# Kernel optimization log

Hardware: AMD Instinct MI355X
Metric: run time of the kernel (lower is better)

The kernel has to match this reference:

```python
import jax, jax.numpy as jnp
import numpy as np
import math

B, S, DIM = 32, 1, 4096
NH, NKV, HD = 32, 8, 128
MAXLEN = 4096
START_POS = 4095


def _rope(t, freqs):
    # t: (b, s, h, hd); freqs: (s, hd//2, 2) = (cos/real, sin/imag)
    b, s, h, hd = t.shape
    tr = t.astype(jnp.float32).reshape(b, s, h, hd // 2, 2)
    c = freqs[None, :, None, :, 0]
    sn = freqs[None, :, None, :, 1]
    x0, x1 = tr[..., 0], tr[..., 1]
    out = jnp.stack([x0 * c - x1 * sn, x0 * sn + x1 * c], axis=-1)
    return out.reshape(b, s, h, hd).astype(t.dtype)


def setup_inputs() -> dict:
    key = jax.random.key(0)
    ks = jax.random.split(key, 8)
    sd = 1.0 / math.sqrt(DIM)
    x = jax.random.normal(ks[0], (B, S, DIM), dtype=jnp.float32)
    freqs = jax.random.normal(ks[1], (S, HD // 2, 2), dtype=jnp.float32)
    cache_k = jax.random.normal(ks[2], (B, MAXLEN, NKV, HD), dtype=jnp.float32)
    cache_v = jax.random.normal(ks[3], (B, MAXLEN, NKV, HD), dtype=jnp.float32)
    wq = jax.random.normal(ks[4], (NH * HD, DIM), dtype=jnp.float32) * sd
    wk = jax.random.normal(ks[5], (NKV * HD, DIM), dtype=jnp.float32) * sd
    wv = jax.random.normal(ks[6], (NKV * HD, DIM), dtype=jnp.float32) * sd
    wo = jax.random.normal(ks[7], (DIM, NH * HD), dtype=jnp.float32) * sd
    return {"x": x, "freqs": freqs, "cache_k": cache_k, "cache_v": cache_v,
            "wq": wq, "wk": wk, "wv": wv, "wo": wo, "start_pos": START_POS}


def reference(x, freqs, cache_k, cache_v, wq, wk, wv, wo, start_pos):
    b, s, _ = x.shape
    n_rep = NH // NKV
    xq = (x @ wq.T).reshape(b, s, NH, HD)
    xk = (x @ wk.T).reshape(b, s, NKV, HD)
    xv = (x @ wv.T).reshape(b, s, NKV, HD)
    xq = _rope(xq, freqs)
    xk = _rope(xk, freqs)
    # KV-cache write then read of prefix (static start_pos)
    keys = cache_k.at[:, start_pos:start_pos + s].set(xk)[:, :start_pos + s]
    values = cache_v.at[:, start_pos:start_pos + s].set(xv)[:, :start_pos + s]
    # GQA: group q heads (g=NKV kv groups, r=n_rep) without materializing repeat
    q = xq.reshape(b, s, NKV, n_rep, HD)
    scores = jnp.einsum('bsgrd,blgd->bgrsl', q, keys) / math.sqrt(HD)
    probs = jax.nn.softmax(scores.astype(jnp.float32), axis=-1).astype(xq.dtype)
    out = jnp.einsum('bgrsl,blgd->bsgrd', probs, values).reshape(b, s, NH * HD)
    return out @ wo.T
```

## Files before the change

kernel.cpp:

```cpp
#include <hip/hip_runtime.h>

#define QSCALE 0.08838834764831845f


#define GEMM_FMA(r, wf) \
    acc[r][0] = fmaf(wf.x, x0.x, acc[r][0]); acc[r][0] = fmaf(wf.y, x0.y, acc[r][0]); \
    acc[r][0] = fmaf(wf.z, x0.z, acc[r][0]); acc[r][0] = fmaf(wf.w, x0.w, acc[r][0]); \
    acc[r][1] = fmaf(wf.x, x1.x, acc[r][1]); acc[r][1] = fmaf(wf.y, x1.y, acc[r][1]); \
    acc[r][1] = fmaf(wf.z, x1.z, acc[r][1]); acc[r][1] = fmaf(wf.w, x1.w, acc[r][1]); \
    acc[r][2] = fmaf(wf.x, x2.x, acc[r][2]); acc[r][2] = fmaf(wf.y, x2.y, acc[r][2]); \
    acc[r][2] = fmaf(wf.z, x2.z, acc[r][2]); acc[r][2] = fmaf(wf.w, x2.w, acc[r][2]); \
    acc[r][3] = fmaf(wf.x, x3.x, acc[r][3]); acc[r][3] = fmaf(wf.y, x3.y, acc[r][3]); \
    acc[r][3] = fmaf(wf.z, x3.z, acc[r][3]); acc[r][3] = fmaf(wf.w, x3.w, acc[r][3]);

__device__ __forceinline__ void gemv3(
    const float* __restrict__ W,
    const float* __restrict__ X,
    float* __restrict__ part, const int M, const int m0, const int ks)
{
    const int t = threadIdx.x;
    const int ksub = t & 3;
    const int ngrp = (t >> 2) & 7;
    const int mgrp = t >> 5;

    const int kbase = ks * 256 + ksub * 4;
    const float* wr0 = W + (size_t)(mgrp * 8 + 0) * 4096 + kbase;
    const float* wr1 = W + (size_t)(mgrp * 8 + 1) * 4096 + kbase;
    const float* wr2 = W + (size_t)(mgrp * 8 + 2) * 4096 + kbase;
    const float* wr3 = W + (size_t)(mgrp * 8 + 3) * 4096 + kbase;
    const float* wr4 = W + (size_t)(mgrp * 8 + 4) * 4096 + kbase;
    const float* wr5 = W + (size_t)(mgrp * 8 + 5) * 4096 + kbase;
    const float* wr6 = W + (size_t)(mgrp * 8 + 6) * 4096 + kbase;
    const float* wr7 = W + (size_t)(mgrp * 8 + 7) * 4096 + kbase;
    const float* xr0 = X + (size_t)(ngrp * 4 + 0) * 4096 + kbase;
    const float* xr1 = X + (size_t)(ngrp * 4 + 1) * 4096 + kbase;
    const float* xr2 = X + (size_t)(ngrp * 4 + 2) * 4096 + kbase;
    const float* xr3 = X + (size_t)(ngrp * 4 + 3) * 4096 + kbase;

    float acc[8][4];
#pragma unroll
    for (int r = 0; r < 8; ++r)
#pragma unroll
        for (int n = 0; n < 4; ++n) acc[r][n] = 0.f;

#pragma unroll 2
    for (int c = 0; c < 16; ++c) {
        const int off = c * 16;
        const float4 w0 = *(const float4*)(wr0 + off);
        const float4 w1 = *(const float4*)(wr1 + off);
        const float4 w2 = *(const float4*)(wr2 + off);
        const float4 w3 = *(const float4*)(wr3 + off);
        const float4 w4 = *(const float4*)(wr4 + off);
        const float4 w5 = *(const float4*)(wr5 + off);
        const float4 w6 = *(const float4*)(wr6 + off);
        const float4 w7 = *(const float4*)(wr7 + off);
        const float4 x0 = *(const float4*)(xr0 + off);
        const float4 x1 = *(const float4*)(xr1 + off);
        const float4 x2 = *(const float4*)(xr2 + off);
        const float4 x3 = *(const float4*)(xr3 + off);
        GEMM_FMA(0, w0) GEMM_FMA(1, w1) GEMM_FMA(2, w2) GEMM_FMA(3, w3)
        GEMM_FMA(4, w4) GEMM_FMA(5, w5) GEMM_FMA(6, w6) GEMM_FMA(7, w7)
    }

#pragma unroll
    for (int r = 0; r < 8; ++r)
#pragma unroll
        for (int n = 0; n < 4; ++n) {
            acc[r][n] += __shfl_xor(acc[r][n], 1);
            acc[r][n] += __shfl_xor(acc[r][n], 2);
        }

    if (ksub == 0) {
        float* base = part + (size_t)ks * 32 * M + m0 + mgrp * 8;
#pragma unroll
        for (int n = 0; n < 4; ++n) {
            float* dst = base + (size_t)(ngrp * 4 + n) * M;
            *(float4*)(dst)     = make_float4(acc[0][n], acc[1][n], acc[2][n], acc[3][n]);
            *(float4*)(dst + 4) = make_float4(acc[4][n], acc[5][n], acc[6][n], acc[7][n]);
        }
    }
}

__global__ __launch_bounds__(256, 4) void gemv_qkv_kernel(
    const float* __restrict__ wq, const float* __restrict__ wk,
    const float* __restrict__ wv, const float* __restrict__ x,
    float* __restrict__ part)
{
    const int mb = blockIdx.x >> 4, ks = blockIdx.x & 15;
    const int m0 = mb * 64;
    const float* W;
    if (m0 < 4096)      W = wq + (size_t)m0 * 4096;
    else if (m0 < 5120) W = wk + (size_t)(m0 - 4096) * 4096;
    else                W = wv + (size_t)(m0 - 5120) * 4096;
    gemv3(W, x, part, 6144, m0, ks);
}

__global__ __launch_bounds__(256, 4) void gemv_out_kernel(
    const float* __restrict__ wo, const float* __restrict__ a_ws,
    float* __restrict__ part)
{
    const int mb = blockIdx.x >> 4, ks = blockIdx.x & 15;
    gemv3(wo + (size_t)(mb * 64) * 4096, a_ws, part, 4096, mb * 64, ks);
}

__global__ __launch_bounds__(256) void qkv_combine_kernel(
    const float* __restrict__ part,
    const float* __restrict__ freqs,
    float* __restrict__ qc_g, float* __restrict__ kn_g, float* __restrict__ vn_g)
{
    const int idx = blockIdx.x * 256 + threadIdx.x;
    const int b = idx / 1536;
    const int cm = (idx - b * 1536) * 4;
    const float* p = part + (size_t)b * 6144 + cm;
    float4 v = make_float4(0.f, 0.f, 0.f, 0.f);
#pragma unroll
    for (int s = 0; s < 16; ++s) {
        const float4 a = *(const float4*)(p + (size_t)s * (32 * 6144));
        v.x += a.x; v.y += a.y; v.z += a.z; v.w += a.w;
    }
    if (cm < 4096) {
        const int d = cm & 127;
        const float4 f = *(const float4*)(freqs + d);
        float4 o;
        o.x = (v.x * f.x - v.y * f.y) * QSCALE;
        o.y = (v.x * f.y + v.y * f.x) * QSCALE;
        o.z = (v.z * f.z - v.w * f.w) * QSCALE;
        o.w = (v.z * f.w + v.w * f.z) * QSCALE;
        *(float4*)(qc_g + (size_t)b * 4096 + cm) = o;
    } else if (cm < 5120) {
        const int d = (cm - 4096) & 127;
        const float4 f = *(const float4*)(freqs + d);
        float4 o;
        o.x = v.x * f.x - v.y * f.y;
        o.y = v.x * f.y + v.y * f.x;
        o.z = v.z * f.z - v.w * f.w;
        o.w = v.z * f.w + v.w * f.z;
        *(float4*)(kn_g + (size_t)b * 1024 + (cm - 4096)) = o;
    } else {
        *(float4*)(vn_g + (size_t)b * 1024 + (cm - 5120)) = v;
    }
}

__global__ __launch_bounds__(512, 2) void attn3_kernel(
    const float* __restrict__ qc_g, const float* __restrict__ kn_g,
    const float* __restrict__ vn_g,
    const float* __restrict__ cache_k, const float* __restrict__ cache_v,
    float* __restrict__ pmss, float* __restrict__ pacc)
{
    const int t = threadIdx.x;
    const int wave = t >> 6, lane = t & 63;
    const int g8 = lane >> 3, j = lane & 7;
    const int b = blockIdx.x >> 3, split = blockIdx.x & 7;
    const int base = split * 512 + wave * 64;

    float4 q[4][4];
    const float* qb = qc_g + (size_t)b * 4096 + g8 * 512 + j * 4;
#pragma unroll
    for (int h = 0; h < 4; ++h)
#pragma unroll
        for (int p = 0; p < 4; ++p)
            q[h][p] = *(const float4*)(qb + h * 128 + p * 32);

    float m[4] = {-1e30f, -1e30f, -1e30f, -1e30f};
    float ss[4] = {0.f, 0.f, 0.f, 0.f};
    float4 acc[4][4];
#pragma unroll
    for (int h = 0; h < 4; ++h)
#pragma unroll
        for (int p = 0; p < 4; ++p) acc[h][p] = make_float4(0.f, 0.f, 0.f, 0.f);

    auto process = [&](const float4* kf, const float4* vf) {
#pragma unroll
        for (int h = 0; h < 4; ++h) {
            float d = 0.f;
#pragma unroll
            for (int p = 0; p < 4; ++p) {
                d = fmaf(q[h][p].x, kf[p].x, d);
                d = fmaf(q[h][p].y, kf[p].y, d);
                d = fmaf(q[h][p].z, kf[p].z, d);
                d = fmaf(q[h][p].w, kf[p].w, d);
            }
            d += __shfl_xor(d, 1);
            d += __shfl_xor(d, 2);
            d += __shfl_xor(d, 4);
            const float dd = d - m[h];
            float pe;
            if (dd > 8.0f) {
                const float c = __expf(-dd);
                ss[h] = fmaf(ss[h], c, 1.0f);
#pragma unroll
                for (int p = 0; p < 4; ++p) {
                    acc[h][p].x *= c; acc[h][p].y *= c;
                    acc[h][p].z *= c; acc[h][p].w *= c;
                }
                m[h] = d; pe = 1.0f;
            } else {
                pe = __expf(dd);
                ss[h] += pe;
            }
#pragma unroll
            for (int p = 0; p < 4; ++p) {
                acc[h][p].x = fmaf(pe, vf[p].x, acc[h][p].x);
                acc[h][p].y = fmaf(pe, vf[p].y, acc[h][p].y);
                acc[h][p].z = fmaf(pe, vf[p].z, acc[h][p].z);
                acc[h][p].w = fmaf(pe, vf[p].w, acc[h][p].w);
            }
        }
    };

    const float* kp = cache_k + ((size_t)b * 4096 + base) * 1024 + g8 * 128 + j * 4;
    const float* vp = cache_v + ((size_t)b * 4096 + base) * 1024 + g8 * 128 + j * 4;

    int nIter = 64;
    if (base + 63 == 4095) {
        nIter = 63;
        float4 kf[4], vf[4];
        const float* kn = kn_g + (size_t)b * 1024 + g8 * 128 + j * 4;
        const float* vn = vn_g + (size_t)b * 1024 + g8 * 128 + j * 4;
#pragma unroll
        for (int p = 0; p < 4; ++p) {
            kf[p] = *(const float4*)(kn + p * 32);
            vf[p] = *(const float4*)(vn + p * 32);
        }
        process(kf, vf);
    }

    float4 ka[4], va[4], kb[4], vb[4];
#pragma unroll
    for (int p = 0; p < 4; ++p) {
        ka[p] = *(const float4*)(kp + p * 32);
        va[p] = *(const float4*)(vp + p * 32);
    }
    int i = 0;
    for (; i + 2 <= nIter; i += 2) {
        const float* k1 = kp + (size_t)(i + 1) * 1024;
        const float* v1 = vp + (size_t)(i + 1) * 1024;
#pragma unroll
        for (int p = 0; p < 4; ++p) {
            kb[p] = *(const float4*)(k1 + p * 32);
            vb[p] = *(const float4*)(v1 + p * 32);
        }
        process(ka, va);
        if (i + 2 < nIter) {
            const float* k2 = kp + (size_t)(i + 2) * 1024;
            const float* v2 = vp + (size_t)(i + 2) * 1024;
#pragma unroll
            for (int p = 0; p < 4; ++p) {
                ka[p] = *(const float4*)(k2 + p * 32);
                va[p] = *(const float4*)(v2 + p * 32);
            }
        }
        process(kb, vb);
    }
    if (i < nIter) process(ka, va);

    const int pidx = ((b * 8 + split) * 8 + wave) * 32 + g8 * 4;
#pragma unroll
    for (int h = 0; h < 4; ++h) {
        float* pr = pacc + (size_t)(pidx + h) * 128 + j * 4;
#pragma unroll
        for (int p = 0; p < 4; ++p)
            *(float4*)(pr + p * 32) = acc[h][p];
    }
    if (j == 0) {
#pragma unroll
        for (int h = 0; h < 4; ++h) {
            pmss[(size_t)(pidx + h) * 2]     = m[h];
            pmss[(size_t)(pidx + h) * 2 + 1] = ss[h];
        }
    }
}

__global__ __launch_bounds__(128) void attn_combine_kernel(
    const float* __restrict__ pmss, const float* __restrict__ pacc,
    float* __restrict__ a_ws)
{
    const int bg = blockIdx.x, t = threadIdx.x;
    const int h = t >> 5, jj = t & 31;
    const int b = bg >> 3, g = bg & 7;

    float M = -1e30f;
#pragma unroll
    for (int sw = 0; sw < 64; ++sw) {
        const int idx = (bg * 8 + (sw >> 3)) * 8 * 32 - bg * 8 * 32 * 8 + 0;
        (void)idx;
    }
#pragma unroll
    for (int s = 0; s < 8; ++s)
#pragma unroll
        for (int w = 0; w < 8; ++w) {
            const int idx = (((b * 8 + s) * 8) + w) * 32 + g * 4 + h;
            M = fmaxf(M, pmss[(size_t)idx * 2]);
        }
    float SS = 0.f;
    float4 o = make_float4(0.f, 0.f, 0.f, 0.f);
#pragma unroll
    for (int s = 0; s < 8; ++s)
#pragma unroll
        for (int w = 0; w < 8; ++w) {
            const int idx = (((b * 8 + s) * 8) + w) * 32 + g * 4 + h;
            const float wgt = __expf(pmss[(size_t)idx * 2] - M);
            SS = fmaf(pmss[(size_t)idx * 2 + 1], wgt, SS);
            const float4 a = *(const float4*)(pacc + (size_t)idx * 128 + jj * 4);
            o.x = fmaf(a.x, wgt, o.x);
            o.y = fmaf(a.y, wgt, o.y);
            o.z = fmaf(a.z, wgt, o.z);
            o.w = fmaf(a.w, wgt, o.w);
        }
    const float inv = 1.f / SS;
    o.x *= inv; o.y *= inv; o.z *= inv; o.w *= inv;
    *(float4*)(a_ws + (size_t)b * 4096 + (size_t)(g * 4 + h) * 128 + jj * 4) = o;
}

__global__ __launch_bounds__(256) void out_combine_kernel(
    const float* __restrict__ part, float* __restrict__ out)
{
    const int i4 = (blockIdx.x * 256 + threadIdx.x) * 4;
    float4 v = make_float4(0.f, 0.f, 0.f, 0.f);
#pragma unroll
    for (int s = 0; s < 16; ++s) {
        const float4 a = *(const float4*)(part + (size_t)s * 131072 + i4);
        v.x += a.x; v.y += a.y; v.z += a.z; v.w += a.w;
    }
    *(float4*)(out + i4) = v;
}

extern "C" void kernel_launch(void* const* d_in, const int* in_sizes, int n_in,
                              void* d_out, int out_size, void* d_ws, size_t ws_size,
                              hipStream_t stream)
{
    const float* x       = (const float*)d_in[0];
    const float* freqs   = (const float*)d_in[1];
    const float* cache_k = (const float*)d_in[2];
    const float* cache_v = (const float*)d_in[3];
    const float* wq      = (const float*)d_in[4];
    const float* wk      = (const float*)d_in[5];
    const float* wv      = (const float*)d_in[6];
    const float* wo      = (const float*)d_in[7];

    float* out = (float*)d_out;
    float* ws  = (float*)d_ws;
    float* part_qkv = ws;
    float* qc_g     = ws + 3145728;
    float* kn_g     = ws + 3276800;
    float* vn_g     = ws + 3309568;
    float* pmss     = ws + 3342336;
    float* pacc     = ws + 3473408;
    float* a_ws     = ws + 11862016;
    float* part_out = ws + 11993088;

    gemv_qkv_kernel<<<1536, 256, 0, stream>>>(wq, wk, wv, x, part_qkv);
    qkv_combine_kernel<<<192, 256, 0, stream>>>(part_qkv, freqs, qc_g, kn_g, vn_g);
    attn3_kernel<<<256, 512, 0, stream>>>(qc_g, kn_g, vn_g, cache_k, cache_v, pmss, pacc);
    attn_combine_kernel<<<256, 128, 0, stream>>>(pmss, pacc, a_ws);
    gemv_out_kernel<<<1024, 256, 0, stream>>>(wo, a_ws, part_out);
    out_combine_kernel<<<128, 256, 0, stream>>>(part_out, out);
}
```

Baseline: 350.2 us.

## Remap attention decode so each wave handles two KV groups over 128 rows

Restructures the attention kernel so each 32-lane half-wave owns one KV group and covers the full 128-wide head dimension with one float4 per lane. Each wave then walks 128 cache rows instead of 64. The grid grows to 1024 blocks of 256 threads, and the sequence is split into 16x2 chunks instead of 8x8. Per-thread register state (q, accumulators) shrinks fourfold to raise occupancy, and the partial-result buffers and combine loops shrink from 64 to 32 partials per head. In exchange, the dot-product reduction needs 5 shuffle stages instead of 3, and each load is a single float4 per row with a deeper per-row prefetch chain.

New measurement: 330.8 us. 5.5% less time.

```diff
diff --git a/kernel.cpp b/kernel.cpp
--- a/kernel.cpp
+++ b/kernel.cpp
@@ -141,127 +141,96 @@
     }
 }
 
-__global__ __launch_bounds__(512, 2) void attn3_kernel(
+__global__ __launch_bounds__(256, 4) void attn4_kernel(
     const float* __restrict__ qc_g, const float* __restrict__ kn_g,
     const float* __restrict__ vn_g,
     const float* __restrict__ cache_k, const float* __restrict__ cache_v,
     float* __restrict__ pmss, float* __restrict__ pacc)
 {
     const int t = threadIdx.x;
-    const int wave = t >> 6, lane = t & 63;
-    const int g8 = lane >> 3, j = lane & 7;
-    const int b = blockIdx.x >> 3, split = blockIdx.x & 7;
-    const int base = split * 512 + wave * 64;
-
-    float4 q[4][4];
-    const float* qb = qc_g + (size_t)b * 4096 + g8 * 512 + j * 4;
-#pragma unroll
-    for (int h = 0; h < 4; ++h)
-#pragma unroll
-        for (int p = 0; p < 4; ++p)
-            q[h][p] = *(const float4*)(qb + h * 128 + p * 32);
-
-    float m[4] = {-1e30f, -1e30f, -1e30f, -1e30f};
+    const int w = t >> 6, lane = t & 63;
+    const int g2 = lane >> 5, j = lane & 31;
+    const int bid = blockIdx.x;
+    const int q2 = bid & 1, split = (bid >> 1) & 15, b = bid >> 5;
+    const int gsub = w >> 1, rsub = w & 1;
+    const int g = q2 * 4 + gsub * 2 + g2;
+    const int row0 = split * 256 + rsub * 128;
+
+    float4 q[4];
+    const float* qb = qc_g + (size_t)b * 4096 + (size_t)g * 512 + j * 4;
+#pragma unroll
+    for (int h = 0; h < 4; ++h) q[h] = *(const float4*)(qb + h * 128);
+
+    float m[4]  = {-1e30f, -1e30f, -1e30f, -1e30f};
     float ss[4] = {0.f, 0.f, 0.f, 0.f};
-    float4 acc[4][4];
-#pragma unroll
-    for (int h = 0; h < 4; ++h)
-#pragma unroll
-        for (int p = 0; p < 4; ++p) acc[h][p] = make_float4(0.f, 0.f, 0.f, 0.f);
-
-    auto process = [&](const float4* kf, const float4* vf) {
+    float4 acc[4];
+#pragma unroll
+    for (int h = 0; h < 4; ++h) acc[h] = make_float4(0.f, 0.f, 0.f, 0.f);
+
+    auto process = [&](const float4 kf, const float4 vf) {
+        float d[4];
+#pragma unroll
+        for (int h = 0; h < 4; ++h)
+            d[h] = fmaf(q[h].x, kf.x, fmaf(q[h].y, kf.y,
+                   fmaf(q[h].z, kf.z, q[h].w * kf.w)));
+#pragma unroll
+        for (int mask = 1; mask <= 16; mask <<= 1) {
+            d[0] += __shfl_xor(d[0], mask);
+            d[1] += __shfl_xor(d[1], mask);
+            d[2] += __shfl_xor(d[2], mask);
+            d[3] += __shfl_xor(d[3], mask);
+        }
 #pragma unroll
         for (int h = 0; h < 4; ++h) {
-            float d = 0.f;
-#pragma unroll
-            for (int p = 0; p < 4; ++p) {
-                d = fmaf(q[h][p].x, kf[p].x, d);
-                d = fmaf(q[h][p].y, kf[p].y, d);
-                d = fmaf(q[h][p].z, kf[p].z, d);
-                d = fmaf(q[h][p].w, kf[p].w, d);
-            }
-            d += __shfl_xor(d, 1);
-            d += __shfl_xor(d, 2);
-            d += __shfl_xor(d, 4);
-            const float dd = d - m[h];
+            const float dd = d[h] - m[h];
             float pe;
             if (dd > 8.0f) {
                 const float c = __expf(-dd);
                 ss[h] = fmaf(ss[h], c, 1.0f);
-#pragma unroll
-                for (int p = 0; p < 4; ++p) {
-                    acc[h][p].x *= c; acc[h][p].y *= c;
-                    acc[h][p].z *= c; acc[h][p].w *= c;
-                }
-                m[h] = d; pe = 1.0f;
+                acc[h].x *= c; acc[h].y *= c; acc[h].z *= c; acc[h].w *= c;
+                m[h] = d[h]; pe = 1.0f;
             } else {
                 pe = __expf(dd);
                 ss[h] += pe;
             }
-#pragma unroll
-            for (int p = 0; p < 4; ++p) {
-                acc[h][p].x = fmaf(pe, vf[p].x, acc[h][p].x);
-                acc[h][p].y = fmaf(pe, vf[p].y, acc[h][p].y);
-                acc[h][p].z = fmaf(pe, vf[p].z, acc[h][p].z);
-                acc[h][p].w = fmaf(pe, vf[p].w, acc[h][p].w);
-            }
+            acc[h].x = fmaf(pe, vf.x, acc[h].x);
+            acc[h].y = fmaf(pe, vf.y, acc[h].y);
+            acc[h].z = fmaf(pe, vf.z, acc[h].z);
+            acc[h].w = fmaf(pe, vf.w, acc[h].w);
         }
     };
 
-    const float* kp = cache_k + ((size_t)b * 4096 + base) * 1024 + g8 * 128 + j * 4;
-    const float* vp = cache_v + ((size_t)b * 4096 + base) * 1024 + g8 * 128 + j * 4;
-
-    int nIter = 64;
-    if (base + 63 == 4095) {
-        nIter = 63;
-        float4 kf[4], vf[4];
-        const float* kn = kn_g + (size_t)b * 1024 + g8 * 128 + j * 4;
-        const float* vn = vn_g + (size_t)b * 1024 + g8 * 128 + j * 4;
-#pragma unroll
-        for (int p = 0; p < 4; ++p) {
-            kf[p] = *(const float4*)(kn + p * 32);
-            vf[p] = *(const float4*)(vn + p * 32);
-        }
+    const size_t cbase = ((size_t)b * 4096 + row0) * 1024 + (size_t)g * 128 + j * 4;
+    const float* kp = cache_k + cbase;
+    const float* vp = cache_v + cbase;
+
+    const bool lastw = (split == 15) && (rsub == 1);
+    const int n = lastw ? 127 : 128;
+
+    float4 kA = *(const float4*)(kp);
+    float4 vA = *(const float4*)(vp);
+    float4 kB = *(const float4*)(kp + 1024);
+    float4 vB = *(const float4*)(vp + 1024);
+#pragma unroll 2
+    for (int i = 0; i < n; ++i) {
+        float4 kC, vC;
+        if (i + 2 < n) {
+            kC = *(const float4*)(kp + (size_t)(i + 2) * 1024);
+            vC = *(const float4*)(vp + (size_t)(i + 2) * 1024);
+        }
+        process(kA, vA);
+        kA = kB; vA = vB; kB = kC; vB = vC;
+    }
+    if (lastw) {
+        const float4 kf = *(const float4*)(kn_g + (size_t)b * 1024 + (size_t)g * 128 + j * 4);
+        const float4 vf = *(const float4*)(vn_g + (size_t)b * 1024 + (size_t)g * 128 + j * 4);
         process(kf, vf);
     }
 
-    float4 ka[4], va[4], kb[4], vb[4];
-#pragma unroll
-    for (int p = 0; p < 4; ++p) {
-        ka[p] = *(const float4*)(kp + p * 32);
-        va[p] = *(const float4*)(vp + p * 32);
-    }
-    int i = 0;
-    for (; i + 2 <= nIter; i += 2) {
-        const float* k1 = kp + (size_t)(i + 1) * 1024;
-        const float* v1 = vp + (size_t)(i + 1) * 1024;
-#pragma unroll
-        for (int p = 0; p < 4; ++p) {
-            kb[p] = *(const float4*)(k1 + p * 32);
-            vb[p] = *(const float4*)(v1 + p * 32);
-        }
-        process(ka, va);
-        if (i + 2 < nIter) {
-            const float* k2 = kp + (size_t)(i + 2) * 1024;
-            const float* v2 = vp + (size_t)(i + 2) * 1024;
-#pragma unroll
-            for (int p = 0; p < 4; ++p) {
-                ka[p] = *(const float4*)(k2 + p * 32);
-                va[p] = *(const float4*)(v2 + p * 32);
-            }
-        }
-        process(kb, vb);
-    }
-    if (i < nIter) process(ka, va);
-
-    const int pidx = ((b * 8 + split) * 8 + wave) * 32 + g8 * 4;
-#pragma unroll
-    for (int h = 0; h < 4; ++h) {
-        float* pr = pacc + (size_t)(pidx + h) * 128 + j * 4;
-#pragma unroll
-        for (int p = 0; p < 4; ++p)
-            *(float4*)(pr + p * 32) = acc[h][p];
-    }
+    const int pidx = (((b * 16 + split) * 2 + rsub) * 8 + g) * 4;
+#pragma unroll
+    for (int h = 0; h < 4; ++h)
+        *(float4*)(pacc + (size_t)(pidx + h) * 128 + j * 4) = acc[h];
     if (j == 0) {
 #pragma unroll
         for (int h = 0; h < 4; ++h) {
@@ -281,24 +250,19 @@
 
     float M = -1e30f;
 #pragma unroll
-    for (int sw = 0; sw < 64; ++sw) {
-        const int idx = (bg * 8 + (sw >> 3)) * 8 * 32 - bg * 8 * 32 * 8 + 0;
-        (void)idx;
-    }
-#pragma unroll
-    for (int s = 0; s < 8; ++s)
-#pragma unroll
-        for (int w = 0; w < 8; ++w) {
-            const int idx = (((b * 8 + s) * 8) + w) * 32 + g * 4 + h;
+    for (int s = 0; s < 16; ++s)
+#pragma unroll
+        for (int r = 0; r < 2; ++r) {
+            const int idx = (((b * 16 + s) * 2 + r) * 8 + g) * 4 + h;
             M = fmaxf(M, pmss[(size_t)idx * 2]);
         }
     float SS = 0.f;
     float4 o = make_float4(0.f, 0.f, 0.f, 0.f);
 #pragma unroll
-    for (int s = 0; s < 8; ++s)
-#pragma unroll
-        for (int w = 0; w < 8; ++w) {
-            const int idx = (((b * 8 + s) * 8) + w) * 32 + g * 4 + h;
+    for (int s = 0; s < 16; ++s)
+#pragma unroll
+        for (int r = 0; r < 2; ++r) {
+            const int idx = (((b * 16 + s) * 2 + r) * 8 + g) * 4 + h;
             const float wgt = __expf(pmss[(size_t)idx * 2] - M);
             SS = fmaf(pmss[(size_t)idx * 2 + 1], wgt, SS);
             const float4 a = *(const float4*)(pacc + (size_t)idx * 128 + jj * 4);
@@ -345,13 +309,13 @@
     float* kn_g     = ws + 3276800;
     float* vn_g     = ws + 3309568;
     float* pmss     = ws + 3342336;
-    float* pacc     = ws + 3473408;
-    float* a_ws     = ws + 11862016;
-    float* part_out = ws + 11993088;
+    float* pacc     = ws + 3407872;
+    float* a_ws     = ws + 7602176;
+    float* part_out = ws + 7733248;
 
     gemv_qkv_kernel<<<1536, 256, 0, stream>>>(wq, wk, wv, x, part_qkv);
     qkv_combine_kernel<<<192, 256, 0, stream>>>(part_qkv, freqs, qc_g, kn_g, vn_g);
-    attn3_kernel<<<256, 512, 0, stream>>>(qc_g, kn_g, vn_g, cache_k, cache_v, pmss, pacc);
+    attn4_kernel<<<1024, 256, 0, stream>>>(qc_g, kn_g, vn_g, cache_k, cache_v, pmss, pacc);
     attn_combine_kernel<<<256, 128, 0, stream>>>(pmss, pacc, a_ws);
     gemv_out_kernel<<<1024, 256, 0, stream>>>(wo, a_ws, part_out);
     out_combine_kernel<<<128, 256, 0, stream>>>(part_out, out);
```
